# Optimization experiments

Hardware: AMD Instinct MI355X
Metric: run time of the kernel (lower is better)

Reference implementation:

```python
import jax, jax.numpy as jnp
from jax import lax
import numpy as np

T, B, D, H = 2048, 32, 256, 256

def setup_inputs() -> dict:
    key = jax.random.key(0)
    ks = jax.random.split(key, 8)
    inp = {
        'input_': jax.random.normal(ks[0], (T, B, D), dtype=jnp.float32),
        'length': jax.random.randint(ks[1], (B,), 0, T, dtype=jnp.int64),
        'Wih0': jax.random.normal(ks[2], (D, 3 * H), dtype=jnp.float32) * 0.05,
        'Whh0': jax.random.normal(ks[3], (H, 3 * H), dtype=jnp.float32) * 0.05,
        'b0': jax.random.normal(ks[4], (3 * H,), dtype=jnp.float32) * 0.05,
        'Wih1': jax.random.normal(ks[5], (H, 3 * H), dtype=jnp.float32) * 0.05,
        'Whh1': jax.random.normal(ks[6], (H, 3 * H), dtype=jnp.float32) * 0.05,
        'b1': jax.random.normal(ks[7], (3 * H,), dtype=jnp.float32) * 0.05,
    }
    return inp


def _run_layer(x, length, Wih, Whh, b, h0):
    # x: [T, B, D_in]; scan over time with hidden state carried on-chip.
    def step(h, xs):
        x_t, t_idx = xs
        pre = h @ Whh + x_t @ Wih + b          # [B, 3H]
        h_pre, t_pre, _c_pre = jnp.split(pre, 3, axis=1)
        t_gate = jax.nn.sigmoid(t_pre)
        c_gate = jax.nn.sigmoid(t_gate)         # bug-faithful: sigmoid of sigmoid(t_pre)
        s_t = jnp.tanh(h_pre) * t_gate + h * c_gate
        mask = (t_idx < length)[:, None]         # [B, 1]
        h_next = jnp.where(mask, s_t, h)
        return h_next, h_next
    times = jnp.arange(x.shape[0])
    h_n, out = lax.scan(step, h0, (x, times))
    return out, h_n


def reference(input_, length, Wih0, Whh0, b0, Wih1, Whh1, b1):
    h0 = jnp.zeros((input_.shape[1], H), dtype=input_.dtype)
    out0, hn0 = _run_layer(input_, length, Wih0, Whh0, b0, h0)
    # dropout=0 -> identity between layers; each layer reuses the same zero h_0
    out1, hn1 = _run_layer(out0, length, Wih1, Whh1, b1, h0)
    h_n = jnp.stack([hn0, hn1], axis=0)          # [num_layers, B, H]
    return out1, h_n
```

## Files before the change

kernel.cpp:

```cpp
#include <hip/hip_runtime.h>
#include <cstdint>
#include <cstddef>

static constexpr int T_STEPS = 2048;
static constexpr int BATCH   = 32;
static constexpr int DIM     = 256;
static constexpr int NCOL    = 512;
static constexpr int RB      = 16;
static constexpr size_t M_ROWS = (size_t)T_STEPS * BATCH;

typedef _Float16 f16x4 __attribute__((ext_vector_type(4)));
typedef _Float16 f16x8 __attribute__((ext_vector_type(8)));
typedef float    f32x4 __attribute__((ext_vector_type(4)));
struct alignas(8) H4 { _Float16 x, y, z, w; };

static constexpr size_t XW_OFF   = 0;
static constexpr size_t A_OFF    = M_ROWS * NCOL * 2;
static constexpr size_t BLOB_OFF = A_OFF + M_ROWS * DIM * 2;
static constexpr size_t BLOB_ELT = (size_t)DIM * NCOL;
static constexpr size_t FLAG_OFF = BLOB_OFF + 4 * BLOB_ELT * 2;

__global__ void cvt_f32_to_f16(const float* __restrict__ src, _Float16* __restrict__ dst,
                               int n4, int* __restrict__ flags) {
  if (blockIdx.x == 0 && threadIdx.x < 128) flags[threadIdx.x] = 0;
  int i = blockIdx.x * blockDim.x + threadIdx.x;
  if (i >= n4) return;
  float4 v = ((const float4*)src)[i];
  H4 o; o.x = (_Float16)v.x; o.y = (_Float16)v.y; o.z = (_Float16)v.z; o.w = (_Float16)v.w;
  ((H4*)dst)[i] = o;
}

__global__ void prep_blobs4(const float* __restrict__ w0, const float* __restrict__ w1,
                            const float* __restrict__ w2, const float* __restrict__ w3,
                            _Float16* __restrict__ blobs) {
  int gid = blockIdx.x * blockDim.x + threadIdx.x;
  int mat = gid >> 17;
  int rem = gid & 131071;
  int k = rem >> 9;
  int n = rem & 511;
  const float* src = (mat == 0) ? w0 : (mat == 1) ? w1 : (mat == 2) ? w2 : w3;
  float v = src[k * 768 + n];
  int kc = k >> 5, q = (k >> 3) & 3, j = k & 7, tn = n >> 4;
  int lane = (n & 15) + 16 * q;
  blobs[(size_t)mat * BLOB_ELT + ((size_t)(tn * 8 + kc) * 64 + lane) * 8 + j] = (_Float16)v;
}

__global__ __launch_bounds__(256) void gemm_xw(const _Float16* __restrict__ A,
                                               const _Float16* __restrict__ blob,
                                               const float* __restrict__ bias,
                                               _Float16* __restrict__ XW) {
  int lane = threadIdx.x & 63;
  int wave = threadIdx.x >> 6;
  int wid  = blockIdx.x * 4 + wave;
  int mbase = (wid >> 1) * 16;
  int nhalf = wid & 1;
  int q = lane >> 4, n15 = lane & 15;

  f32x4 acc[16];
#pragma unroll
  for (int i = 0; i < 16; i++) acc[i] = (f32x4){0.f, 0.f, 0.f, 0.f};

  const _Float16* Arow = A + (size_t)(mbase + n15) * DIM + q * 8;
#pragma unroll
  for (int kc = 0; kc < 8; kc++) {
    f16x8 af = *(const f16x8*)(Arow + kc * 32);
#pragma unroll
    for (int nt = 0; nt < 16; nt++) {
      const _Float16* bp = blob + ((size_t)((nhalf * 16 + nt) * 8 + kc) * 64 + lane) * 8;
      f16x8 bf = *(const f16x8*)bp;
      acc[nt] = __builtin_amdgcn_mfma_f32_16x16x32_f16(af, bf, acc[nt], 0, 0, 0);
    }
  }
#pragma unroll
  for (int nt = 0; nt < 16; nt++) {
    int col = nhalf * 256 + nt * 16 + n15;
    float bv = bias[col];
#pragma unroll
    for (int r = 0; r < 4; r++) {
      int m = mbase + q * 4 + r;
      XW[(size_t)m * NCOL + col] = (_Float16)(acc[nt][r] + bv);
    }
  }
}

__device__ __forceinline__ int read_len(const void* p, int b) {
  const long long* q = (const long long*)p;
  bool ok64 = true;
  for (int i = 0; i < 32; i++) { long long v = q[i]; if (v < 0 || v > 2048) ok64 = false; }
  return ok64 ? (int)q[b] : ((const int*)p)[b];
}

__device__ __forceinline__ void gload_lds_row(const _Float16* g, _Float16* l) {
  __builtin_amdgcn_global_load_lds(
      (const __attribute__((address_space(1))) void*)g,
      (__attribute__((address_space(3))) void*)l, 16, 0, 0);
}

__device__ __forceinline__ void gate_update(float pre_h, float pre_t, bool live, float& h) {
  const float K1 = 1.442695040888963f, K2 = 2.885390081777927f;
  float phc = fminf(fmaxf(pre_h, -20.f), 20.f);
  float e1 = __builtin_amdgcn_exp2f(-K2 * phc);
  float e2 = __builtin_amdgcn_exp2f(-K1 * pre_t);
  float u1 = 1.f + e1;
  float rr = __builtin_amdgcn_rcpf(u1 * (1.f + e2));
  float ttg = (1.f - e1) * rr;
  float tg  = u1 * rr;
  float cg = 0.5f + tg * (0.250905f + tg * (-0.00432f + tg * (-0.015525f)));
  float s = ttg + h * cg;
  h = live ? s : h;
}

__global__ __launch_bounds__(512, 2) void recur_fused(const _Float16* __restrict__ xw0,
                                                      const _Float16* __restrict__ bwhh0,
                                                      const _Float16* __restrict__ bwhh1,
                                                      const _Float16* __restrict__ bwih1,
                                                      const float* __restrict__ b1,
                                                      const void* __restrict__ lenp,
                                                      _Float16* __restrict__ xw1ring,
                                                      float* __restrict__ out1,
                                                      float* __restrict__ hn,
                                                      int* __restrict__ flags) {
  const int bid  = blockIdx.x;
  const int tid  = threadIdx.x;
  const int w    = tid >> 6;
  const int lane = tid & 63;
  const int q = lane >> 4, l15 = lane & 15;
  int* cons_flags = flags + 64;

  __shared__ __align__(16) _Float16 hbuf[2][DIM];
  __shared__ __align__(16) _Float16 xbuf[2][16][NCOL];
  __shared__ __align__(16) _Float16 sbuf[2][16][DIM];

  const int c0 = (2 * w) * 16 + l15;
  const int c1 = (2 * w + 1) * 16 + l15;
  constexpr int NB = T_STEPS / 16;

  if (bid < BATCH) {
    const int b = bid;
    const int len = read_len(lenp, b);
    f16x8 Bh[2][8], Bt[2][8];
#pragma unroll
    for (int pp = 0; pp < 2; pp++)
#pragma unroll
      for (int kc = 0; kc < 8; kc++) {
        Bh[pp][kc] = *(const f16x8*)(bwhh0 + ((size_t)((2 * w + pp) * 8 + kc) * 64 + lane) * 8);
        Bt[pp][kc] = *(const f16x8*)(bwhh0 + ((size_t)((16 + 2 * w + pp) * 8 + kc) * 64 + lane) * 8);
      }
    const float bb0 = b1[c0], bb1 = b1[c1], bb2 = b1[c0 + 256], bb3 = b1[c1 + 256];
    if (tid < DIM) hbuf[0][tid] = (_Float16)0.f;

    const _Float16* xrow = xw0 + (size_t)b * NCOL;
    const size_t xstride = (size_t)BATCH * NCOL;

    gload_lds_row(xrow + (size_t)(2 * w)     * xstride + lane * 8, &xbuf[0][2 * w][0]);
    gload_lds_row(xrow + (size_t)(2 * w + 1) * xstride + lane * 8, &xbuf[0][2 * w + 1][0]);
    asm volatile("s_waitcnt vmcnt(0)" ::: "memory");
    __syncthreads();

    float h0 = 0.f, h1 = 0.f;
    int cons_seen = 0;
    for (int tb = 0; tb < NB; ++tb) {
      const int buf = tb & 1;
      if (tb + 1 < NB) {
        const _Float16* gsrc = xrow + (size_t)((tb + 1) * 16) * xstride;
        gload_lds_row(gsrc + (size_t)(2 * w)     * xstride + lane * 8, &xbuf[1 - buf][2 * w][0]);
        gload_lds_row(gsrc + (size_t)(2 * w + 1) * xstride + lane * 8, &xbuf[1 - buf][2 * w + 1][0]);
      }
#pragma unroll
      for (int ts = 0; ts < 16; ++ts) {
        const int t = tb * 16 + ts;
        const int p = ts & 1;
        const _Float16* xr = &xbuf[buf][ts][0];
        const float xh0 = (float)xr[c0],       xh1 = (float)xr[c1];
        const float xt0 = (float)xr[c0 + 256], xt1 = (float)xr[c1 + 256];

        f32x4 a0 = {0.f, 0.f, 0.f, 0.f}, a1 = a0, a2 = a0, a3 = a0;
        const _Float16* hb = &hbuf[p][q * 8];
#pragma unroll
        for (int kc = 0; kc < 8; kc++) {
          f16x8 a = *(const f16x8*)(hb + kc * 32);
          a0 = __builtin_amdgcn_mfma_f32_16x16x32_f16(a, Bh[0][kc], a0, 0, 0, 0);
          a1 = __builtin_amdgcn_mfma_f32_16x16x32_f16(a, Bh[1][kc], a1, 0, 0, 0);
          a2 = __builtin_amdgcn_mfma_f32_16x16x32_f16(a, Bt[0][kc], a2, 0, 0, 0);
          a3 = __builtin_amdgcn_mfma_f32_16x16x32_f16(a, Bt[1][kc], a3, 0, 0, 0);
        }
        const bool live = t < len;
        gate_update(a0[0] + xh0, a2[0] + xt0, live, h0);
        gate_update(a1[0] + xh1, a3[0] + xt1, live, h1);
        _Float16 s0 = (_Float16)h0, s1 = (_Float16)h1;
        if (q == 0) {
          hbuf[1 - p][c0] = s0;
          hbuf[1 - p][c1] = s1;
          char* sb = (char*)&sbuf[buf][0][0];
          const int sw = (ts & 7) << 4;
          *(_Float16*)(sb + ((ts * 512 + c0 * 2) ^ sw)) = s0;
          *(_Float16*)(sb + ((ts * 512 + c1 * 2) ^ sw)) = s1;
        }
        if (ts == 15) {
          asm volatile("s_waitcnt vmcnt(0) lgkmcnt(0)\n\ts_barrier" ::: "memory");
        } else {
          asm volatile("s_waitcnt lgkmcnt(0)\n\ts_barrier" ::: "memory");
        }
      }
      if (tb - cons_seen >= RB - 2) {
        int it = 0;
        while ((cons_seen = __hip_atomic_load(&cons_flags[b], __ATOMIC_RELAXED,
                                              __HIP_MEMORY_SCOPE_AGENT)) < tb - (RB - 2)) {
          __builtin_amdgcn_s_sleep(2);
          if (++it > (1 << 22)) break;
        }
      }
      {
        const char* sb = (const char*)&sbuf[buf][0][0];
        f16x8 xa_[8];
#pragma unroll
        for (int kc = 0; kc < 8; kc++) {
          const int off_ = (l15 * 512 + q * 16 + kc * 64) ^ ((l15 & 7) << 4);
          xa_[kc] = *(const f16x8*)(sb + off_);
        }
        _Float16* dst = xw1ring + (size_t)(b * RB + (tb & (RB - 1))) * 16 * NCOL;
#pragma unroll
        for (int ti = 0; ti < 4; ti++) {
          const int tn = (ti < 2) ? (2 * w + ti) : (16 + 2 * w + (ti - 2));
          f32x4 acc = {0.f, 0.f, 0.f, 0.f};
#pragma unroll
          for (int kc = 0; kc < 8; kc++) {
            f16x8 bf = *(const f16x8*)(bwih1 + ((size_t)(tn * 8 + kc) * 64 + lane) * 8);
            acc = __builtin_amdgcn_mfma_f32_16x16x32_f16(xa_[kc], bf, acc, 0, 0, 0);
          }
          const int   col = (ti == 0) ? c0 : (ti == 1) ? c1 : (ti == 2) ? (c0 + 256)
                                                                        : (c1 + 256);
          const float bv  = (ti == 0) ? bb0 : (ti == 1) ? bb1 : (ti == 2) ? bb2 : bb3;
#pragma unroll
          for (int r2 = 0; r2 < 4; r2++)
            dst[(size_t)(q * 4 + r2) * NCOL + col] = (_Float16)(acc[r2] + bv);
        }
      }
      if ((tb & 3) == 3) {
        asm volatile("s_waitcnt vmcnt(0) lgkmcnt(0)\n\ts_barrier" ::: "memory");
        if (tid == 0)
          __hip_atomic_store(&flags[b], tb + 1, __ATOMIC_RELEASE, __HIP_MEMORY_SCOPE_AGENT);
      } else {
        asm volatile("s_waitcnt lgkmcnt(0)\n\ts_barrier" ::: "memory");
      }
    }
    if (q == 0) {
      hn[b * DIM + c0] = h0;
      hn[b * DIM + c1] = h1;
    }
  } else {
    const int b = bid - BATCH;
    const int len = read_len(lenp, b);
    f16x8 Bh[2][8], Bt[2][8];
#pragma unroll
    for (int pp = 0; pp < 2; pp++)
#pragma unroll
      for (int kc = 0; kc < 8; kc++) {
        Bh[pp][kc] = *(const f16x8*)(bwhh1 + ((size_t)((2 * w + pp) * 8 + kc) * 64 + lane) * 8);
        Bt[pp][kc] = *(const f16x8*)(bwhh1 + ((size_t)((16 + 2 * w + pp) * 8 + kc) * 64 + lane) * 8);
      }
    if (tid < DIM) hbuf[0][tid] = (_Float16)0.f;
    __syncthreads();

#define WAIT_FLAG(TH_, ACQ_)                                                             \
    {                                                                                    \
      int it = 0;                                                                        \
      while (__hip_atomic_load(&flags[b], __ATOMIC_RELAXED, __HIP_MEMORY_SCOPE_AGENT)    \
             < (TH_)) {                                                                  \
        __builtin_amdgcn_s_sleep(2);                                                     \
        if (++it > (1 << 22)) break;           \
      }                                                                                  \
      if (ACQ_)                                                                          \
        (void)__hip_atomic_load(&flags[b], __ATOMIC_ACQUIRE, __HIP_MEMORY_SCOPE_AGENT);  \
    }

#define STAGE_RING(TB_, NB_)                                                             \
    {                                                                                    \
      const _Float16* base =                                                             \
          xw1ring + (size_t)(b * RB + ((TB_) & (RB - 1))) * 16 * NCOL;                   \
      gload_lds_row(base + (size_t)(2 * w)     * NCOL + lane * 8, &xbuf[NB_][2 * w][0]); \
      gload_lds_row(base + (size_t)(2 * w + 1) * NCOL + lane * 8, &xbuf[NB_][2 * w + 1][0]); \
    }

    float h0 = 0.f, h1 = 0.f;

    WAIT_FLAG(1, true);
    STAGE_RING(0, 0);
    asm volatile("s_waitcnt vmcnt(0)" ::: "memory");
    __syncthreads();

    for (int tb = 0; tb < NB; ++tb) {
      const int buf = tb & 1;
      if (tb + 1 < NB) {
        WAIT_FLAG(tb + 2, ((tb + 2) & 3) == 1);
        STAGE_RING(tb + 1, 1 - buf);
      }
#pragma unroll
      for (int ts = 0; ts < 16; ++ts) {
        const int t = tb * 16 + ts;
        const int p = ts & 1;
        const _Float16* xr = &xbuf[buf][ts][0];
        const float xh0 = (float)xr[c0],       xh1 = (float)xr[c1];
        const float xt0 = (float)xr[c0 + 256], xt1 = (float)xr[c1 + 256];

        f32x4 a0 = {0.f, 0.f, 0.f, 0.f}, a1 = a0, a2 = a0, a3 = a0;
        const _Float16* hb = &hbuf[p][q * 8];
#pragma unroll
        for (int kc = 0; kc < 8; kc++) {
          f16x8 a = *(const f16x8*)(hb + kc * 32);
          a0 = __builtin_amdgcn_mfma_f32_16x16x32_f16(a, Bh[0][kc], a0, 0, 0, 0);
          a1 = __builtin_amdgcn_mfma_f32_16x16x32_f16(a, Bh[1][kc], a1, 0, 0, 0);
          a2 = __builtin_amdgcn_mfma_f32_16x16x32_f16(a, Bt[0][kc], a2, 0, 0, 0);
          a3 = __builtin_amdgcn_mfma_f32_16x16x32_f16(a, Bt[1][kc], a3, 0, 0, 0);
        }
        const bool live = t < len;
        gate_update(a0[0] + xh0, a2[0] + xt0, live, h0);
        gate_update(a1[0] + xh1, a3[0] + xt1, live, h1);
        if (q == 0) {
          hbuf[1 - p][c0] = (_Float16)h0;
          hbuf[1 - p][c1] = (_Float16)h1;
          size_t o = ((size_t)t * BATCH + b) * DIM;
          out1[o + c0] = h0; out1[o + c1] = h1;
        }
        if (ts == 15) {
          asm volatile("s_waitcnt vmcnt(0) lgkmcnt(0)\n\ts_barrier" ::: "memory");
        } else {
          asm volatile("s_waitcnt lgkmcnt(0)\n\ts_barrier" ::: "memory");
        }
      }
      if (((tb & 3) == 3) && tid == 0)
        __hip_atomic_store(&cons_flags[b], tb + 1, __ATOMIC_RELAXED, __HIP_MEMORY_SCOPE_AGENT);
    }
#undef STAGE_RING
#undef WAIT_FLAG
    if (q == 0) {
      hn[BATCH * DIM + b * DIM + c0] = h0;
      hn[BATCH * DIM + b * DIM + c1] = h1;
    }
  }
}

extern "C" void kernel_launch(void* const* d_in, const int* in_sizes, int n_in,
                              void* d_out, int out_size, void* d_ws, size_t ws_size,
                              hipStream_t stream) {
  const float* input_ = (const float*)d_in[0];
  const void*  lenp   = d_in[1];
  const float* Wih0   = (const float*)d_in[2];
  const float* Whh0   = (const float*)d_in[3];
  const float* b0     = (const float*)d_in[4];
  const float* Wih1   = (const float*)d_in[5];
  const float* Whh1   = (const float*)d_in[6];
  const float* b1     = (const float*)d_in[7];
  float* out = (float*)d_out;
  char*  ws  = (char*)d_ws;

  _Float16* XW    = (_Float16*)(ws + XW_OFF);
  _Float16* Abuf  = (_Float16*)(ws + A_OFF);
  _Float16* blobs = (_Float16*)(ws + BLOB_OFF);
  int*      flags = (int*)(ws + FLAG_OFF);
  float* hn = out + M_ROWS * DIM;

  cvt_f32_to_f16<<<16384, 256, 0, stream>>>(input_, Abuf, (int)(M_ROWS * DIM / 4), flags);
  prep_blobs4<<<2048, 256, 0, stream>>>(Wih0, Wih1, Whh0, Whh1, blobs);
  gemm_xw<<<2048, 256, 0, stream>>>(Abuf, blobs + 0 * BLOB_ELT, b0, XW);
  recur_fused<<<2 * BATCH, 512, 0, stream>>>(XW,
                                             blobs + 2 * BLOB_ELT,
                                             blobs + 3 * BLOB_ELT,
                                             blobs + 1 * BLOB_ELT,
                                             b1, lenp,
                                             Abuf,
                                             out, hn, flags);
}
```

Baseline: 2.436 ms.

## Offload layer-1 input GEMM to dedicated extra waves in producer blocks

Block size grows from 512 to 768 threads. The 4 extra waves in each layer-0 block compute the layer-1 input projection (x·Wih1 + b1) for the previous 16-step chunk, running alongside the recurrent waves instead of stalling them at every chunk boundary. The helper waves take part in the per-step barriers and wait on the consumer flags, while the recurrent waves no longer block on ring backpressure. In the consumer blocks the extra waves sit idle apart from barriers. The cost is more register pressure under the wider launch bound and extra barrier participants on the critical recurrent path.

```diff
diff --git a/kernel.cpp b/kernel.cpp
--- a/kernel.cpp
+++ b/kernel.cpp
@@ -110,7 +110,7 @@
   h = live ? s : h;
 }
 
-__global__ __launch_bounds__(512, 2) void recur_fused(const _Float16* __restrict__ xw0,
+__global__ __launch_bounds__(768, 2) void recur_fused(const _Float16* __restrict__ xw0,
                                                       const _Float16* __restrict__ bwhh0,
                                                       const _Float16* __restrict__ bwhh1,
                                                       const _Float16* __restrict__ bwih1,
@@ -126,139 +126,159 @@
   const int lane = tid & 63;
   const int q = lane >> 4, l15 = lane & 15;
   int* cons_flags = flags + 64;
+  const bool recw = (w < 8);
 
   __shared__ __align__(16) _Float16 hbuf[2][DIM];
   __shared__ __align__(16) _Float16 xbuf[2][16][NCOL];
   __shared__ __align__(16) _Float16 sbuf[2][16][DIM];
 
-  const int c0 = (2 * w) * 16 + l15;
-  const int c1 = (2 * w + 1) * 16 + l15;
+  const int c0 = (recw ? (2 * w) * 16 : 0) + l15;
+  const int c1 = (recw ? (2 * w + 1) * 16 : 16) + l15;
   constexpr int NB = T_STEPS / 16;
 
   if (bid < BATCH) {
     const int b = bid;
     const int len = read_len(lenp, b);
-    f16x8 Bh[2][8], Bt[2][8];
-#pragma unroll
-    for (int pp = 0; pp < 2; pp++)
-#pragma unroll
-      for (int kc = 0; kc < 8; kc++) {
-        Bh[pp][kc] = *(const f16x8*)(bwhh0 + ((size_t)((2 * w + pp) * 8 + kc) * 64 + lane) * 8);
-        Bt[pp][kc] = *(const f16x8*)(bwhh0 + ((size_t)((16 + 2 * w + pp) * 8 + kc) * 64 + lane) * 8);
-      }
-    const float bb0 = b1[c0], bb1 = b1[c1], bb2 = b1[c0 + 256], bb3 = b1[c1 + 256];
-    if (tid < DIM) hbuf[0][tid] = (_Float16)0.f;
-
-    const _Float16* xrow = xw0 + (size_t)b * NCOL;
-    const size_t xstride = (size_t)BATCH * NCOL;
-
-    gload_lds_row(xrow + (size_t)(2 * w)     * xstride + lane * 8, &xbuf[0][2 * w][0]);
-    gload_lds_row(xrow + (size_t)(2 * w + 1) * xstride + lane * 8, &xbuf[0][2 * w + 1][0]);
-    asm volatile("s_waitcnt vmcnt(0)" ::: "memory");
-    __syncthreads();
-
-    float h0 = 0.f, h1 = 0.f;
-    int cons_seen = 0;
-    for (int tb = 0; tb < NB; ++tb) {
-      const int buf = tb & 1;
-      if (tb + 1 < NB) {
-        const _Float16* gsrc = xrow + (size_t)((tb + 1) * 16) * xstride;
-        gload_lds_row(gsrc + (size_t)(2 * w)     * xstride + lane * 8, &xbuf[1 - buf][2 * w][0]);
-        gload_lds_row(gsrc + (size_t)(2 * w + 1) * xstride + lane * 8, &xbuf[1 - buf][2 * w + 1][0]);
-      }
-#pragma unroll
-      for (int ts = 0; ts < 16; ++ts) {
-        const int t = tb * 16 + ts;
-        const int p = ts & 1;
-        const _Float16* xr = &xbuf[buf][ts][0];
-        const float xh0 = (float)xr[c0],       xh1 = (float)xr[c1];
-        const float xt0 = (float)xr[c0 + 256], xt1 = (float)xr[c1 + 256];
-
-        f32x4 a0 = {0.f, 0.f, 0.f, 0.f}, a1 = a0, a2 = a0, a3 = a0;
-        const _Float16* hb = &hbuf[p][q * 8];
+
+    if (recw) {
+      f16x8 Bh[2][8], Bt[2][8];
+#pragma unroll
+      for (int pp = 0; pp < 2; pp++)
 #pragma unroll
         for (int kc = 0; kc < 8; kc++) {
-          f16x8 a = *(const f16x8*)(hb + kc * 32);
-          a0 = __builtin_amdgcn_mfma_f32_16x16x32_f16(a, Bh[0][kc], a0, 0, 0, 0);
-          a1 = __builtin_amdgcn_mfma_f32_16x16x32_f16(a, Bh[1][kc], a1, 0, 0, 0);
-          a2 = __builtin_amdgcn_mfma_f32_16x16x32_f16(a, Bt[0][kc], a2, 0, 0, 0);
-          a3 = __builtin_amdgcn_mfma_f32_16x16x32_f16(a, Bt[1][kc], a3, 0, 0, 0);
-        }
-        const bool live = t < len;
-        gate_update(a0[0] + xh0, a2[0] + xt0, live, h0);
-        gate_update(a1[0] + xh1, a3[0] + xt1, live, h1);
-        _Float16 s0 = (_Float16)h0, s1 = (_Float16)h1;
-        if (q == 0) {
-          hbuf[1 - p][c0] = s0;
-          hbuf[1 - p][c1] = s1;
-          char* sb = (char*)&sbuf[buf][0][0];
-          const int sw = (ts & 7) << 4;
-          *(_Float16*)(sb + ((ts * 512 + c0 * 2) ^ sw)) = s0;
-          *(_Float16*)(sb + ((ts * 512 + c1 * 2) ^ sw)) = s1;
-        }
-        if (ts == 15) {
-          asm volatile("s_waitcnt vmcnt(0) lgkmcnt(0)\n\ts_barrier" ::: "memory");
-        } else {
+          Bh[pp][kc] = *(const f16x8*)(bwhh0 + ((size_t)((2 * w + pp) * 8 + kc) * 64 + lane) * 8);
+          Bt[pp][kc] = *(const f16x8*)(bwhh0 + ((size_t)((16 + 2 * w + pp) * 8 + kc) * 64 + lane) * 8);
+        }
+      if (tid < DIM) hbuf[0][tid] = (_Float16)0.f;
+
+      const _Float16* xrow = xw0 + (size_t)b * NCOL;
+      const size_t xstride = (size_t)BATCH * NCOL;
+
+      gload_lds_row(xrow + (size_t)(2 * w)     * xstride + lane * 8, &xbuf[0][2 * w][0]);
+      gload_lds_row(xrow + (size_t)(2 * w + 1) * xstride + lane * 8, &xbuf[0][2 * w + 1][0]);
+      asm volatile("s_waitcnt vmcnt(0)" ::: "memory");
+      __syncthreads();
+
+      float h0 = 0.f, h1 = 0.f;
+      for (int tb = 0; tb < NB; ++tb) {
+        const int buf = tb & 1;
+        if (tb + 1 < NB) {
+          const _Float16* gsrc = xrow + (size_t)((tb + 1) * 16) * xstride;
+          gload_lds_row(gsrc + (size_t)(2 * w)     * xstride + lane * 8, &xbuf[1 - buf][2 * w][0]);
+          gload_lds_row(gsrc + (size_t)(2 * w + 1) * xstride + lane * 8, &xbuf[1 - buf][2 * w + 1][0]);
+        }
+#pragma unroll
+        for (int ts = 0; ts < 16; ++ts) {
+          const int t = tb * 16 + ts;
+          const int p = ts & 1;
+          const _Float16* xr = &xbuf[buf][ts][0];
+          const float xh0 = (float)xr[c0],       xh1 = (float)xr[c1];
+          const float xt0 = (float)xr[c0 + 256], xt1 = (float)xr[c1 + 256];
+
+          f32x4 a0 = {0.f, 0.f, 0.f, 0.f}, a1 = a0, a2 = a0, a3 = a0;
+          const _Float16* hb = &hbuf[p][q * 8];
+#pragma unroll
+          for (int kc = 0; kc < 8; kc++) {
+            f16x8 a = *(const f16x8*)(hb + kc * 32);
+            a0 = __builtin_amdgcn_mfma_f32_16x16x32_f16(a, Bh[0][kc], a0, 0, 0, 0);
+            a1 = __builtin_amdgcn_mfma_f32_16x16x32_f16(a, Bh[1][kc], a1, 0, 0, 0);
+            a2 = __builtin_amdgcn_mfma_f32_16x16x32_f16(a, Bt[0][kc], a2, 0, 0, 0);
+            a3 = __builtin_amdgcn_mfma_f32_16x16x32_f16(a, Bt[1][kc], a3, 0, 0, 0);
+          }
+          const bool live = t < len;
+          gate_update(a0[0] + xh0, a2[0] + xt0, live, h0);
+          gate_update(a1[0] + xh1, a3[0] + xt1, live, h1);
+          _Float16 s0 = (_Float16)h0, s1 = (_Float16)h1;
+          if (q == 0) {
+            hbuf[1 - p][c0] = s0;
+            hbuf[1 - p][c1] = s1;
+            char* sb = (char*)&sbuf[buf][0][0];
+            const int sw = (ts & 7) << 4;
+            *(_Float16*)(sb + ((ts * 512 + c0 * 2) ^ sw)) = s0;
+            *(_Float16*)(sb + ((ts * 512 + c1 * 2) ^ sw)) = s1;
+          }
+          if (ts == 15) {
+            asm volatile("s_waitcnt vmcnt(0) lgkmcnt(0)\n\ts_barrier" ::: "memory");
+          } else {
+            asm volatile("s_waitcnt lgkmcnt(0)\n\ts_barrier" ::: "memory");
+          }
+        }
+      }
+      if (q == 0) {
+        hn[b * DIM + c0] = h0;
+        hn[b * DIM + c1] = h1;
+      }
+    } else {
+      const int wx = w - 8;
+      float bb[8];
+#pragma unroll
+      for (int i = 0; i < 8; i++) bb[i] = b1[(wx * 8 + i) * 16 + l15];
+      __syncthreads();
+
+      int cons_seen = 0;
+#define XGEMM_BLOCK(TBM1_)                                                               \
+      {                                                                                  \
+        const int pbuf_ = (TBM1_) & 1;                                                   \
+                              \
+        if ((TBM1_) - cons_seen >= RB - 2) {                                             \
+          int it = 0;                                                                    \
+          while ((cons_seen = __hip_atomic_load(&cons_flags[b], __ATOMIC_RELAXED,        \
+                                                __HIP_MEMORY_SCOPE_AGENT))               \
+                 < (TBM1_) - (RB - 2)) {                                                 \
+            __builtin_amdgcn_s_sleep(2);                                                 \
+            if (++it > (1 << 22)) break;                                                 \
+          }                                                                              \
+        }                                                                                \
+        const char* sb_ = (const char*)&sbuf[pbuf_][0][0];                               \
+        f16x8 xa_[8];                                                                    \
+        _Pragma("unroll")                                                                \
+        for (int kc = 0; kc < 8; kc++) {                                                 \
+          const int off_ = (l15 * 512 + q * 16 + kc * 64) ^ ((l15 & 7) << 4);            \
+          xa_[kc] = *(const f16x8*)(sb_ + off_);                                         \
+        }                                                                                \
+        _Float16* dst_ = xw1ring + (size_t)(b * RB + ((TBM1_) & (RB - 1))) * 16 * NCOL;  \
+        _Pragma("unroll")                                                                \
+        for (int i = 0; i < 8; i++) {                                                    \
+          const int tn_ = wx * 8 + i;                                                    \
+          f32x4 acc = {0.f, 0.f, 0.f, 0.f};                                              \
+          _Pragma("unroll")                                                              \
+          for (int kc = 0; kc < 8; kc++) {                                               \
+            f16x8 bf = *(const f16x8*)(bwih1 + ((size_t)(tn_ * 8 + kc) * 64 + lane) * 8);\
+            acc = __builtin_amdgcn_mfma_f32_16x16x32_f16(xa_[kc], bf, acc, 0, 0, 0);     \
+          }                                                                              \
+          _Pragma("unroll")                                                              \
+          for (int r2 = 0; r2 < 4; r2++)                                                 \
+            dst_[(size_t)(q * 4 + r2) * NCOL + tn_ * 16 + l15] =                         \
+                (_Float16)(acc[r2] + bb[i]);                                             \
+        }                                                                                \
+        asm volatile("s_waitcnt vmcnt(0)" ::: "memory");         \
+        if ((((TBM1_) & 3) == 3) && wx == 0 && lane == 0)                                \
+          __hip_atomic_store(&flags[b], (TBM1_) + 1, __ATOMIC_RELEASE,                   \
+                             __HIP_MEMORY_SCOPE_AGENT);                                  \
+      }
+
+      for (int tb = 0; tb < NB; ++tb) {
+        if (tb > 0) XGEMM_BLOCK(tb - 1);
+        for (int ts = 0; ts < 16; ++ts)
           asm volatile("s_waitcnt lgkmcnt(0)\n\ts_barrier" ::: "memory");
-        }
-      }
-      if (tb - cons_seen >= RB - 2) {
-        int it = 0;
-        while ((cons_seen = __hip_atomic_load(&cons_flags[b], __ATOMIC_RELAXED,
-                                              __HIP_MEMORY_SCOPE_AGENT)) < tb - (RB - 2)) {
-          __builtin_amdgcn_s_sleep(2);
-          if (++it > (1 << 22)) break;
-        }
-      }
-      {
-        const char* sb = (const char*)&sbuf[buf][0][0];
-        f16x8 xa_[8];
-#pragma unroll
-        for (int kc = 0; kc < 8; kc++) {
-          const int off_ = (l15 * 512 + q * 16 + kc * 64) ^ ((l15 & 7) << 4);
-          xa_[kc] = *(const f16x8*)(sb + off_);
-        }
-        _Float16* dst = xw1ring + (size_t)(b * RB + (tb & (RB - 1))) * 16 * NCOL;
-#pragma unroll
-        for (int ti = 0; ti < 4; ti++) {
-          const int tn = (ti < 2) ? (2 * w + ti) : (16 + 2 * w + (ti - 2));
-          f32x4 acc = {0.f, 0.f, 0.f, 0.f};
-#pragma unroll
-          for (int kc = 0; kc < 8; kc++) {
-            f16x8 bf = *(const f16x8*)(bwih1 + ((size_t)(tn * 8 + kc) * 64 + lane) * 8);
-            acc = __builtin_amdgcn_mfma_f32_16x16x32_f16(xa_[kc], bf, acc, 0, 0, 0);
-          }
-          const int   col = (ti == 0) ? c0 : (ti == 1) ? c1 : (ti == 2) ? (c0 + 256)
-                                                                        : (c1 + 256);
-          const float bv  = (ti == 0) ? bb0 : (ti == 1) ? bb1 : (ti == 2) ? bb2 : bb3;
-#pragma unroll
-          for (int r2 = 0; r2 < 4; r2++)
-            dst[(size_t)(q * 4 + r2) * NCOL + col] = (_Float16)(acc[r2] + bv);
-        }
-      }
-      if ((tb & 3) == 3) {
-        asm volatile("s_waitcnt vmcnt(0) lgkmcnt(0)\n\ts_barrier" ::: "memory");
-        if (tid == 0)
-          __hip_atomic_store(&flags[b], tb + 1, __ATOMIC_RELEASE, __HIP_MEMORY_SCOPE_AGENT);
-      } else {
-        asm volatile("s_waitcnt lgkmcnt(0)\n\ts_barrier" ::: "memory");
-      }
-    }
-    if (q == 0) {
-      hn[b * DIM + c0] = h0;
-      hn[b * DIM + c1] = h1;
+      }
+      XGEMM_BLOCK(NB - 1);
+#undef XGEMM_BLOCK
     }
   } else {
     const int b = bid - BATCH;
     const int len = read_len(lenp, b);
+    const bool active = recw;
     f16x8 Bh[2][8], Bt[2][8];
-#pragma unroll
-    for (int pp = 0; pp < 2; pp++)
-#pragma unroll
-      for (int kc = 0; kc < 8; kc++) {
-        Bh[pp][kc] = *(const f16x8*)(bwhh1 + ((size_t)((2 * w + pp) * 8 + kc) * 64 + lane) * 8);
-        Bt[pp][kc] = *(const f16x8*)(bwhh1 + ((size_t)((16 + 2 * w + pp) * 8 + kc) * 64 + lane) * 8);
-      }
+    if (active) {
+#pragma unroll
+      for (int pp = 0; pp < 2; pp++)
+#pragma unroll
+        for (int kc = 0; kc < 8; kc++) {
+          Bh[pp][kc] = *(const f16x8*)(bwhh1 + ((size_t)((2 * w + pp) * 8 + kc) * 64 + lane) * 8);
+          Bt[pp][kc] = *(const f16x8*)(bwhh1 + ((size_t)((16 + 2 * w + pp) * 8 + kc) * 64 + lane) * 8);
+        }
+    }
     if (tid < DIM) hbuf[0][tid] = (_Float16)0.f;
     __syncthreads();
 
@@ -268,7 +288,7 @@
       while (__hip_atomic_load(&flags[b], __ATOMIC_RELAXED, __HIP_MEMORY_SCOPE_AGENT)    \
              < (TH_)) {                                                                  \
         __builtin_amdgcn_s_sleep(2);                                                     \
-        if (++it > (1 << 22)) break;           \
+        if (++it > (1 << 22)) break;                                   \
       }                                                                                  \
       if (ACQ_)                                                                          \
         (void)__hip_atomic_load(&flags[b], __ATOMIC_ACQUIRE, __HIP_MEMORY_SCOPE_AGENT);  \
@@ -284,56 +304,61 @@
 
     float h0 = 0.f, h1 = 0.f;
 
-    WAIT_FLAG(1, true);
-    STAGE_RING(0, 0);
-    asm volatile("s_waitcnt vmcnt(0)" ::: "memory");
+    if (active) {
+      WAIT_FLAG(1, true);
+      STAGE_RING(0, 0);
+      asm volatile("s_waitcnt vmcnt(0)" ::: "memory");
+    }
     __syncthreads();
 
     for (int tb = 0; tb < NB; ++tb) {
       const int buf = tb & 1;
-      if (tb + 1 < NB) {
+      if (active && tb + 1 < NB) {
         WAIT_FLAG(tb + 2, ((tb + 2) & 3) == 1);
         STAGE_RING(tb + 1, 1 - buf);
       }
 #pragma unroll
       for (int ts = 0; ts < 16; ++ts) {
-        const int t = tb * 16 + ts;
-        const int p = ts & 1;
-        const _Float16* xr = &xbuf[buf][ts][0];
-        const float xh0 = (float)xr[c0],       xh1 = (float)xr[c1];
-        const float xt0 = (float)xr[c0 + 256], xt1 = (float)xr[c1 + 256];
-
-        f32x4 a0 = {0.f, 0.f, 0.f, 0.f}, a1 = a0, a2 = a0, a3 = a0;
-        const _Float16* hb = &hbuf[p][q * 8];
-#pragma unroll
-        for (int kc = 0; kc < 8; kc++) {
-          f16x8 a = *(const f16x8*)(hb + kc * 32);
-          a0 = __builtin_amdgcn_mfma_f32_16x16x32_f16(a, Bh[0][kc], a0, 0, 0, 0);
-          a1 = __builtin_amdgcn_mfma_f32_16x16x32_f16(a, Bh[1][kc], a1, 0, 0, 0);
-          a2 = __builtin_amdgcn_mfma_f32_16x16x32_f16(a, Bt[0][kc], a2, 0, 0, 0);
-          a3 = __builtin_amdgcn_mfma_f32_16x16x32_f16(a, Bt[1][kc], a3, 0, 0, 0);
-        }
-        const bool live = t < len;
-        gate_update(a0[0] + xh0, a2[0] + xt0, live, h0);
-        gate_update(a1[0] + xh1, a3[0] + xt1, live, h1);
-        if (q == 0) {
-          hbuf[1 - p][c0] = (_Float16)h0;
-          hbuf[1 - p][c1] = (_Float16)h1;
-          size_t o = ((size_t)t * BATCH + b) * DIM;
-          out1[o + c0] = h0; out1[o + c1] = h1;
+        if (active) {
+          const int t = tb * 16 + ts;
+          const int p = ts & 1;
+          const _Float16* xr = &xbuf[buf][ts][0];
+          const float xh0 = (float)xr[c0],       xh1 = (float)xr[c1];
+          const float xt0 = (float)xr[c0 + 256], xt1 = (float)xr[c1 + 256];
+
+          f32x4 a0 = {0.f, 0.f, 0.f, 0.f}, a1 = a0, a2 = a0, a3 = a0;
+          const _Float16* hb = &hbuf[p][q * 8];
+#pragma unroll
+          for (int kc = 0; kc < 8; kc++) {
+            f16x8 a = *(const f16x8*)(hb + kc * 32);
+            a0 = __builtin_amdgcn_mfma_f32_16x16x32_f16(a, Bh[0][kc], a0, 0, 0, 0);
+            a1 = __builtin_amdgcn_mfma_f32_16x16x32_f16(a, Bh[1][kc], a1, 0, 0, 0);
+            a2 = __builtin_amdgcn_mfma_f32_16x16x32_f16(a, Bt[0][kc], a2, 0, 0, 0);
+            a3 = __builtin_amdgcn_mfma_f32_16x16x32_f16(a, Bt[1][kc], a3, 0, 0, 0);
+          }
+          const bool live = t < len;
+          gate_update(a0[0] + xh0, a2[0] + xt0, live, h0);
+          gate_update(a1[0] + xh1, a3[0] + xt1, live, h1);
+          if (q == 0) {
+            hbuf[1 - p][c0] = (_Float16)h0;
+            hbuf[1 - p][c1] = (_Float16)h1;
+            size_t o = ((size_t)t * BATCH + b) * DIM;
+            out1[o + c0] = h0; out1[o + c1] = h1;
+          }
         }
         if (ts == 15) {
-          asm volatile("s_waitcnt vmcnt(0) lgkmcnt(0)\n\ts_barrier" ::: "memory");
+          if (active) asm volatile("s_waitcnt vmcnt(0)" ::: "memory");
+          asm volatile("s_waitcnt lgkmcnt(0)\n\ts_barrier" ::: "memory");
         } else {
           asm volatile("s_waitcnt lgkmcnt(0)\n\ts_barrier" ::: "memory");
         }
       }
-      if (((tb & 3) == 3) && tid == 0)
+      if (active && ((tb & 3) == 3) && tid == 0)
         __hip_atomic_store(&cons_flags[b], tb + 1, __ATOMIC_RELAXED, __HIP_MEMORY_SCOPE_AGENT);
     }
 #undef STAGE_RING
 #undef WAIT_FLAG
-    if (q == 0) {
+    if (active && q == 0) {
       hn[BATCH * DIM + b * DIM + c0] = h0;
       hn[BATCH * DIM + b * DIM + c1] = h1;
     }
@@ -363,7 +388,7 @@
   cvt_f32_to_f16<<<16384, 256, 0, stream>>>(input_, Abuf, (int)(M_ROWS * DIM / 4), flags);
   prep_blobs4<<<2048, 256, 0, stream>>>(Wih0, Wih1, Whh0, Whh1, blobs);
   gemm_xw<<<2048, 256, 0, stream>>>(Abuf, blobs + 0 * BLOB_ELT, b0, XW);
-  recur_fused<<<2 * BATCH, 512, 0, stream>>>(XW,
+  recur_fused<<<2 * BATCH, 768, 0, stream>>>(XW,
                                              blobs + 2 * BLOB_ELT,
                                              blobs + 3 * BLOB_ELT,
                                              blobs + 1 * BLOB_ELT,
```

Result: slower. 3.222 ms (+32.3%).

## Interleave layer-1 input projection of previous block into recurrent timestep loop

Applied to the files above, without the earlier changes.

The layer-0 block producer no longer runs the layer-1 input projection (Wih1 GEMM) as a separate phase after each 16-step block. It spreads the previous block's projection across the 16 timesteps of the current block, two MFMAs per step, so the work can hide behind the latency-bound recurrent chain. A tail handles the last block and publishes the final flag. The cost is a one-block delay in flag publication to the layer-1 consumer, extra register pressure, and an extra global weight load per step. Flag timing also shifts, with stores at tb multiples of 4 rather than after tb%4==3.

```diff
diff --git a/kernel.cpp b/kernel.cpp
--- a/kernel.cpp
+++ b/kernel.cpp
@@ -159,8 +159,28 @@
 
     float h0 = 0.f, h1 = 0.f;
     int cons_seen = 0;
+    f32x4 xacc = {0.f, 0.f, 0.f, 0.f};
     for (int tb = 0; tb < NB; ++tb) {
       const int buf = tb & 1;
+      const bool do_x = (tb > 0);
+      if (do_x && (tb - 1) - cons_seen >= RB - 2) {
+        int it = 0;
+        while ((cons_seen = __hip_atomic_load(&cons_flags[b], __ATOMIC_RELAXED,
+                                              __HIP_MEMORY_SCOPE_AGENT)) < (tb - 1) - (RB - 2)) {
+          __builtin_amdgcn_s_sleep(2);
+          if (++it > (1 << 22)) break;
+        }
+      }
+      f16x8 xa_[8];
+      if (do_x) {
+        const char* sb_ = (const char*)&sbuf[1 - buf][0][0];
+#pragma unroll
+        for (int kc = 0; kc < 8; kc++) {
+          const int off_ = (l15 * 512 + q * 16 + kc * 64) ^ ((l15 & 7) << 4);
+          xa_[kc] = *(const f16x8*)(sb_ + off_);
+        }
+      }
+      _Float16* xdst = xw1ring + (size_t)(b * RB + ((tb - 1) & (RB - 1))) * 16 * NCOL;
       if (tb + 1 < NB) {
         const _Float16* gsrc = xrow + (size_t)((tb + 1) * 16) * xstride;
         gload_lds_row(gsrc + (size_t)(2 * w)     * xstride + lane * 8, &xbuf[1 - buf][2 * w][0]);
@@ -183,6 +203,23 @@
           a1 = __builtin_amdgcn_mfma_f32_16x16x32_f16(a, Bh[1][kc], a1, 0, 0, 0);
           a2 = __builtin_amdgcn_mfma_f32_16x16x32_f16(a, Bt[0][kc], a2, 0, 0, 0);
           a3 = __builtin_amdgcn_mfma_f32_16x16x32_f16(a, Bt[1][kc], a3, 0, 0, 0);
+        }
+        if (do_x) {
+          const int g  = ts >> 2;
+          const int j2 = (ts & 3) * 2;
+          const int tn = (g < 2) ? (2 * w + g) : (16 + 2 * w + (g - 2));
+          f16x8 bf0 = *(const f16x8*)(bwih1 + ((size_t)(tn * 8 + j2) * 64 + lane) * 8);
+          f16x8 bf1 = *(const f16x8*)(bwih1 + ((size_t)(tn * 8 + j2 + 1) * 64 + lane) * 8);
+          if ((ts & 3) == 0) xacc = (f32x4){0.f, 0.f, 0.f, 0.f};
+          xacc = __builtin_amdgcn_mfma_f32_16x16x32_f16(xa_[j2],     bf0, xacc, 0, 0, 0);
+          xacc = __builtin_amdgcn_mfma_f32_16x16x32_f16(xa_[j2 + 1], bf1, xacc, 0, 0, 0);
+          if ((ts & 3) == 3) {
+            const int   col = (g == 0) ? c0 : (g == 1) ? c1 : (g == 2) ? (c0 + 256) : (c1 + 256);
+            const float bv  = (g == 0) ? bb0 : (g == 1) ? bb1 : (g == 2) ? bb2 : bb3;
+#pragma unroll
+            for (int r2 = 0; r2 < 4; r2++)
+              xdst[(size_t)(q * 4 + r2) * NCOL + col] = (_Float16)(xacc[r2] + bv);
+          }
         }
         const bool live = t < len;
         gate_update(a0[0] + xh0, a2[0] + xt0, live, h0);
@@ -202,47 +239,37 @@
           asm volatile("s_waitcnt lgkmcnt(0)\n\ts_barrier" ::: "memory");
         }
       }
-      if (tb - cons_seen >= RB - 2) {
-        int it = 0;
-        while ((cons_seen = __hip_atomic_load(&cons_flags[b], __ATOMIC_RELAXED,
-                                              __HIP_MEMORY_SCOPE_AGENT)) < tb - (RB - 2)) {
-          __builtin_amdgcn_s_sleep(2);
-          if (++it > (1 << 22)) break;
-        }
-      }
-      {
-        const char* sb = (const char*)&sbuf[buf][0][0];
-        f16x8 xa_[8];
+      if (((tb & 3) == 0) && tb > 0 && tid == 0)
+        __hip_atomic_store(&flags[b], tb, __ATOMIC_RELEASE, __HIP_MEMORY_SCOPE_AGENT);
+    }
+    {
+      const char* sb_ = (const char*)&sbuf[(NB - 1) & 1][0][0];
+      f16x8 xa_[8];
+#pragma unroll
+      for (int kc = 0; kc < 8; kc++) {
+        const int off_ = (l15 * 512 + q * 16 + kc * 64) ^ ((l15 & 7) << 4);
+        xa_[kc] = *(const f16x8*)(sb_ + off_);
+      }
+      _Float16* dst = xw1ring + (size_t)(b * RB + ((NB - 1) & (RB - 1))) * 16 * NCOL;
+#pragma unroll
+      for (int ti = 0; ti < 4; ti++) {
+        const int tn = (ti < 2) ? (2 * w + ti) : (16 + 2 * w + (ti - 2));
+        f32x4 acc = {0.f, 0.f, 0.f, 0.f};
 #pragma unroll
         for (int kc = 0; kc < 8; kc++) {
-          const int off_ = (l15 * 512 + q * 16 + kc * 64) ^ ((l15 & 7) << 4);
-          xa_[kc] = *(const f16x8*)(sb + off_);
-        }
-        _Float16* dst = xw1ring + (size_t)(b * RB + (tb & (RB - 1))) * 16 * NCOL;
-#pragma unroll
-        for (int ti = 0; ti < 4; ti++) {
-          const int tn = (ti < 2) ? (2 * w + ti) : (16 + 2 * w + (ti - 2));
-          f32x4 acc = {0.f, 0.f, 0.f, 0.f};
-#pragma unroll
-          for (int kc = 0; kc < 8; kc++) {
-            f16x8 bf = *(const f16x8*)(bwih1 + ((size_t)(tn * 8 + kc) * 64 + lane) * 8);
-            acc = __builtin_amdgcn_mfma_f32_16x16x32_f16(xa_[kc], bf, acc, 0, 0, 0);
-          }
-          const int   col = (ti == 0) ? c0 : (ti == 1) ? c1 : (ti == 2) ? (c0 + 256)
-                                                                        : (c1 + 256);
-          const float bv  = (ti == 0) ? bb0 : (ti == 1) ? bb1 : (ti == 2) ? bb2 : bb3;
-#pragma unroll
-          for (int r2 = 0; r2 < 4; r2++)
-            dst[(size_t)(q * 4 + r2) * NCOL + col] = (_Float16)(acc[r2] + bv);
-        }
-      }
-      if ((tb & 3) == 3) {
-        asm volatile("s_waitcnt vmcnt(0) lgkmcnt(0)\n\ts_barrier" ::: "memory");
-        if (tid == 0)
-          __hip_atomic_store(&flags[b], tb + 1, __ATOMIC_RELEASE, __HIP_MEMORY_SCOPE_AGENT);
-      } else {
-        asm volatile("s_waitcnt lgkmcnt(0)\n\ts_barrier" ::: "memory");
-      }
+          f16x8 bf = *(const f16x8*)(bwih1 + ((size_t)(tn * 8 + kc) * 64 + lane) * 8);
+          acc = __builtin_amdgcn_mfma_f32_16x16x32_f16(xa_[kc], bf, acc, 0, 0, 0);
+        }
+        const int   col = (ti == 0) ? c0 : (ti == 1) ? c1 : (ti == 2) ? (c0 + 256) : (c1 + 256);
+        const float bv  = (ti == 0) ? bb0 : (ti == 1) ? bb1 : (ti == 2) ? bb2 : bb3;
+#pragma unroll
+        for (int r2 = 0; r2 < 4; r2++)
+          dst[(size_t)(q * 4 + r2) * NCOL + col] = (_Float16)(acc[r2] + bv);
+      }
+      asm volatile("s_waitcnt vmcnt(0)" ::: "memory");
+      __syncthreads();
+      if (tid == 0)
+        __hip_atomic_store(&flags[b], NB, __ATOMIC_RELEASE, __HIP_MEMORY_SCOPE_AGENT);
     }
     if (q == 0) {
       hn[b * DIM + c0] = h0;
@@ -268,7 +295,7 @@
       while (__hip_atomic_load(&flags[b], __ATOMIC_RELAXED, __HIP_MEMORY_SCOPE_AGENT)    \
              < (TH_)) {                                                                  \
         __builtin_amdgcn_s_sleep(2);                                                     \
-        if (++it > (1 << 22)) break;           \
+        if (++it > (1 << 22)) break;                                   \
       }                                                                                  \
       if (ACQ_)                                                                          \
         (void)__hip_atomic_load(&flags[b], __ATOMIC_ACQUIRE, __HIP_MEMORY_SCOPE_AGENT);  \
```

After: 2.583 ms. 6.0% more time.
